# Performance work log

Hardware: AMD Instinct MI355X
Metric: run time of the kernel (lower is better)

Reference implementation:

```python
import jax, jax.numpy as jnp
import numpy as np

N = 50000   # total_ent
R = 16      # total_rel
D = 64      # emb_dim
F_IN = 128  # feat_in
L = 2       # gcn_layers
E = 100000  # edges per relation
EPS = 1e-12


def setup_inputs() -> dict:
    key = jax.random.key(0)
    ks = jax.random.split(key, 6)
    x = jax.random.normal(ks[0], (N, F_IN), jnp.float32)
    # xavier-uniform-ish scaled params
    ent_emb = jax.random.normal(ks[1], (F_IN, D), jnp.float32) * (1.0 / np.sqrt(F_IN))
    rel_trans = jax.random.normal(ks[2], (L, R, D, D), jnp.float32) * (1.0 / np.sqrt(D))
    edge_row = jax.random.randint(ks[3], (R, E), 0, N)
    edge_col = jax.random.randint(ks[4], (R, E), 0, N)
    edge_val = jax.random.uniform(ks[5], (R, E), jnp.float32)
    return dict(x=x, ent_emb=ent_emb, rel_trans=rel_trans,
                edge_row=edge_row, edge_col=edge_col, edge_val=edge_val)


def reference(x, ent_emb, rel_trans, edge_row, edge_col, edge_val):
    # emb = x @ ent_emb : [N, D]
    emb = x @ ent_emb

    def spmm_per_rel(emb):
        # per-relation sparse.mm: out[r, row] += val * emb[col]
        def one_rel(row, col, val):
            return jax.ops.segment_sum(val[:, None] * emb[col], row, num_segments=N)
        return jax.vmap(one_rel)(edge_row, edge_col, edge_val)  # [R, N, D]

    for l in range(L):
        emb_acc = spmm_per_rel(emb)                             # [R, N, D]
        # tmp[r] = (W_r @ emb_acc[r]^T)^T = emb_acc[r] @ W_r^T
        tmp = jnp.einsum('rne,rde->rnd', emb_acc, rel_trans[l])  # [R, N, D]
        emb = jax.nn.relu(tmp.sum(axis=0))                       # [N, D]

    # F.normalize(emb) : L2 over dim=1 with eps clamp
    norm = jnp.linalg.norm(emb, axis=1, keepdims=True)
    return emb / jnp.maximum(norm, EPS)
```

## Files before the change

### kernel.cpp

```cpp
#include <hip/hip_runtime.h>

#define Nn 50000
#define Rr 16
#define Dd 64
#define Fin 128
#define Ee 100000
#define NE (Rr * Ee)
#define NBKT 782
#define CB 256
#define EPB (NE / CB)
#define SCTOT (NBKT * CB)
#define SC_NB (SCTOT / 256)
#define NTILE (Nn / 16)

typedef __attribute__((ext_vector_type(8))) short short8;
typedef __attribute__((ext_vector_type(4))) float f32x4;
typedef unsigned short ushort_t;

__device__ inline ushort_t f2bf(float x) {
  union { float f; unsigned u; } v; v.f = x;
  unsigned u = v.u;
  return (ushort_t)((u + 0x7FFFu + ((u >> 16) & 1u)) >> 16);
}
__device__ inline float bf2f(ushort_t h) {
  union { unsigned u; float f; } v; v.u = ((unsigned)h) << 16; return v.f;
}

#define INIT_TILES 3125
#define INIT_NB 782
#define CONVW_NB 512
__global__ __launch_bounds__(256) void pre_k(const float* __restrict__ x,
                                             const float* __restrict__ ent,
                                             ushort_t* __restrict__ emb0,
                                             const float* __restrict__ rel,
                                             ushort_t* __restrict__ wbf,
                                             const int* __restrict__ erow,
                                             int* __restrict__ cnt) {
  __shared__ int lh[NBKT];
  int b = blockIdx.x;
  if (b < INIT_NB) {
    int wave = threadIdx.x >> 6, lane = threadIdx.x & 63;
    int nt = lane & 15, quad = lane >> 4;
    int tile = b * 4 + wave;
    if (tile >= INIT_TILES) return;
    const float* xr = x + ((long)tile * 16 + nt) * Fin + quad * 8;
    short8 afrag[4];
#pragma unroll
    for (int ks = 0; ks < 4; ++ks) {
      float4 p0 = *(const float4*)(xr + ks * 32);
      float4 p1 = *(const float4*)(xr + ks * 32 + 4);
      short8 a;
      a[0] = (short)f2bf(p0.x); a[1] = (short)f2bf(p0.y);
      a[2] = (short)f2bf(p0.z); a[3] = (short)f2bf(p0.w);
      a[4] = (short)f2bf(p1.x); a[5] = (short)f2bf(p1.y);
      a[6] = (short)f2bf(p1.z); a[7] = (short)f2bf(p1.w);
      afrag[ks] = a;
    }
    f32x4 acc[4];
#pragma unroll
    for (int dt = 0; dt < 4; ++dt) acc[dt] = (f32x4){0.f, 0.f, 0.f, 0.f};
#pragma unroll
    for (int ks = 0; ks < 4; ++ks) {
#pragma unroll
      for (int dt = 0; dt < 4; ++dt) {
        short8 bfr;
#pragma unroll
        for (int j = 0; j < 8; ++j)
          bfr[j] = (short)f2bf(ent[(unsigned)(ks * 32 + quad * 8 + j) * Dd + dt * 16 + nt]);
        acc[dt] = __builtin_amdgcn_mfma_f32_16x16x32_bf16(afrag[ks], bfr, acc[dt], 0, 0, 0);
      }
    }
#pragma unroll
    for (int dt = 0; dt < 4; ++dt)
#pragma unroll
      for (int reg = 0; reg < 4; ++reg) {
        int row = tile * 16 + quad * 4 + reg;
        emb0[(unsigned)row * Dd + dt * 16 + nt] = f2bf(acc[dt][reg]);
      }
  } else if (b < INIT_NB + CONVW_NB) {
    int i = (b - INIT_NB) * 256 + threadIdx.x;
    wbf[i] = f2bf(rel[i]);
  } else {
    int blk = b - INIT_NB - CONVW_NB;
    int t = threadIdx.x;
    for (int i = t; i < NBKT; i += 256) lh[i] = 0;
    __syncthreads();
    int r = blk >> 4;
    long gbase = (long)r * Ee + (blk & 15) * EPB;
    for (int i = t; i < EPB; i += 256)
      atomicAdd(&lh[erow[gbase + i] >> 6], 1);
    __syncthreads();
    for (int i = t; i < NBKT; i += 256) cnt[i * CB + blk] = lh[i];
  }
}

__global__ __launch_bounds__(256) void scan1_k(const int* __restrict__ cnt,
                                               int* __restrict__ bsum) {
  __shared__ int ls[256];
  int t = threadIdx.x;
  ls[t] = cnt[blockIdx.x * 256 + t];
  __syncthreads();
  for (int off = 128; off >= 1; off >>= 1) {
    if (t < off) ls[t] += ls[t + off];
    __syncthreads();
  }
  if (t == 0) bsum[blockIdx.x] = ls[0];
}

__global__ __launch_bounds__(1024) void scan2_k(int* __restrict__ bsum) {
  __shared__ int ls[1024];
  int t = threadIdx.x;
  int v = (t < SC_NB) ? bsum[t] : 0;
  ls[t] = v;
  __syncthreads();
  for (int off = 1; off < 1024; off <<= 1) {
    int x = (t >= off) ? ls[t - off] : 0;
    __syncthreads();
    ls[t] += x;
    __syncthreads();
  }
  if (t < SC_NB) bsum[t] = ls[t] - v;
}

__global__ __launch_bounds__(256) void scan3_k(int* __restrict__ cnt,
                                               const int* __restrict__ bsum,
                                               int* __restrict__ cbase,
                                               int* __restrict__ offs) {
  __shared__ int ls[256];
  int t = threadIdx.x, i = blockIdx.x * 256 + t;
  int v = cnt[i];
  ls[t] = v;
  __syncthreads();
  for (int off = 1; off < 256; off <<= 1) {
    int x = (t >= off) ? ls[t - off] : 0;
    __syncthreads();
    ls[t] += x;
    __syncthreads();
  }
  int excl = ls[t] - v + bsum[blockIdx.x];
  cnt[i] = excl;
  if (t == 0) cbase[blockIdx.x] = excl;
  if (i == SCTOT - 1) { cbase[NBKT] = NE; offs[Nn] = NE; }
}

__global__ __launch_bounds__(256) void place_k(const int* __restrict__ erow,
                                               const int* __restrict__ ecol,
                                               const float* __restrict__ ev,
                                               const int* __restrict__ base,
                                               uint2* __restrict__ ebkt) {
  __shared__ int lofs[NBKT];
  int blk = blockIdx.x, t = threadIdx.x;
  for (int i = t; i < NBKT; i += 256) lofs[i] = base[i * CB + blk];
  __syncthreads();
  int r = blk >> 4;
  long gbase = (long)r * Ee + (blk & 15) * EPB;
  for (int i = t; i < EPB; i += 256) {
    long idx = gbase + i;
    int row = erow[idx];
    int pos = atomicAdd(&lofs[row >> 6], 1);
    unsigned vb = f2bf(ev[idx]);
    ebkt[pos] = make_uint2(((unsigned)(row & 63) << 4) | (unsigned)r,
                           (vb << 16) | (unsigned)ecol[idx]);
  }
}

__global__ __launch_bounds__(256) void csort_k(const uint2* __restrict__ ebkt,
                                               const int* __restrict__ cbase,
                                               uint2* __restrict__ ed2,
                                               int* __restrict__ offs) {
  __shared__ int lcnt[64], lstart[64], lcur[64];
  int c = blockIdx.x, t = threadIdx.x;
  int s = cbase[c], e = cbase[c + 1];
  if (t < 64) lcnt[t] = 0;
  __syncthreads();
  for (int i = s + t; i < e; i += 256) atomicAdd(&lcnt[ebkt[i].x >> 4], 1);
  __syncthreads();
  if (t == 0) {
    int run = 0;
    for (int rl = 0; rl < 64; ++rl) {
      int cc = lcnt[rl];
      lstart[rl] = run; lcur[rl] = run; run += cc;
    }
  }
  __syncthreads();
  int nrow = Nn - c * 64; if (nrow > 64) nrow = 64;
  if (t < nrow) offs[c * 64 + t] = s + lstart[t];
  for (int i = s + t; i < e; i += 256) {
    uint2 q = ebkt[i];
    int pos = s + atomicAdd(&lcur[q.x >> 4], 1);
    ed2[pos] = make_uint2(q.x & 15u, q.y);
  }
}

__global__ __launch_bounds__(1024, 8) void fused_k(const ushort_t* __restrict__ emb,
                                                   const int* __restrict__ offs,
                                                   const uint2* __restrict__ ed2,
                                                   const ushort_t* __restrict__ wl,
                                                   ushort_t* __restrict__ embout,
                                                   float* __restrict__ finout,
                                                   int fin) {
  __shared__ ushort_t Zt[16 * 1024];
  __shared__ f32x4 ssred[4][4];
  const int lane = threadIdx.x & 63;
  const int wave = threadIdx.x >> 6;
  const int nt = lane & 15, quad = lane >> 4;
  const int tile = blockIdx.x;

  const int qb = quad << 3;
  const ushort_t* embnt = emb + nt;
  char* ztb = (char*)Zt;
  union AW { unsigned w[4]; short8 v; };

  {
    const int rl = wave;
    const int row = tile * 16 + rl;
    int off_l = (lane < 2) ? offs[row + lane] : 0;
    const int base = __shfl(off_l, 0, 64);
    const int len  = __shfl(off_l, 1, 64) - base;

    f32x4 acc[4];
#pragma unroll
    for (int dt = 0; dt < 4; ++dt) acc[dt] = (f32x4){0.f, 0.f, 0.f, 0.f};

    for (int c = 0; c < len; c += 32) {
      int p = c + (lane & 31);
      uint2 myed = (p < len) ? ed2[base + p] : make_uint2(0u, 0u);

      unsigned yw[4][4];
      unsigned aw[4];
#pragma unroll
      for (int jp = 0; jp < 4; ++jp) {
        unsigned q0 = (unsigned)__shfl((int)myed.y, qb + 2 * jp, 64);
        unsigned q1 = (unsigned)__shfl((int)myed.y, qb + 2 * jp + 1, 64);
        unsigned x0 = (unsigned)__shfl((int)myed.x, qb + 2 * jp, 64);
        unsigned x1 = (unsigned)__shfl((int)myed.x, qb + 2 * jp + 1, 64);
        const ushort_t* e0 = embnt + (q0 & 0xFFFFu) * 64u;
        const ushort_t* e1 = embnt + (q1 & 0xFFFFu) * 64u;
#pragma unroll
        for (int dt = 0; dt < 4; ++dt)
          yw[dt][jp] = (unsigned)e0[dt * 16] | ((unsigned)e1[dt * 16] << 16);
        unsigned t0 = (x0 == (unsigned)nt) ? (q0 >> 16) : 0u;
        unsigned t1 = (x1 == (unsigned)nt) ? (q1 >> 16) : 0u;
        aw[jp] = t0 | (t1 << 16);
      }

      AW af;
      af.w[0] = aw[0]; af.w[1] = aw[1]; af.w[2] = aw[2]; af.w[3] = aw[3];
#pragma unroll
      for (int dt = 0; dt < 4; ++dt) {
        AW bf;
#pragma unroll
        for (int jp = 0; jp < 4; ++jp) bf.w[jp] = yw[dt][jp];
        acc[dt] = __builtin_amdgcn_mfma_f32_16x16x32_bf16(af.v, bf.v, acc[dt], 0, 0, 0);
      }
    }

    const unsigned swz = (unsigned)((rl & 7) << 4);
    const unsigned rb = (unsigned)(rl * 2048 + quad * 512);
#pragma unroll
    for (int dt = 0; dt < 4; ++dt)
#pragma unroll
      for (int reg = 0; reg < 4; ++reg) {
        unsigned hv = (unsigned)f2bf(acc[dt][reg]);
        unsigned pv = (unsigned)__shfl_xor((int)hv, 1, 64);
        if ((nt & 1) == 0) {
          unsigned lg = rb + (unsigned)(reg * 128 + dt * 32 + nt * 2);
          *(unsigned*)(ztb + (lg ^ swz)) = hv | (pv << 16);
        }
      }
  }
  __syncthreads();

  const bool act = (wave < 4);
  f32x4 accO = (f32x4){0.f, 0.f, 0.f, 0.f};
  if (act) {
    const int s0 = nt * 2048 + (((quad    ) ^ (nt & 7)) << 4);
    const int s1 = nt * 2048 + (((quad + 4) ^ (nt & 7)) << 4);
    f32x4 accA = (f32x4){0.f, 0.f, 0.f, 0.f};
    f32x4 accB = (f32x4){0.f, 0.f, 0.f, 0.f};
#pragma unroll
    for (int r = 0; r < 16; r += 2) {
      const char* ab0 = ztb + r * 128;
      const char* ab1 = ztb + (r + 1) * 128;
      short8 a00 = *(const short8*)(ab0 + s0);
      short8 a01 = *(const short8*)(ab0 + s1);
      short8 a10 = *(const short8*)(ab1 + s0);
      short8 a11 = *(const short8*)(ab1 + s1);
      const ushort_t* bp0 = wl + (unsigned)(r * Dd + wave * 16 + nt) * Dd + qb;
      const ushort_t* bp1 = wl + (unsigned)((r + 1) * Dd + wave * 16 + nt) * Dd + qb;
      short8 b00 = *(const short8*)(bp0);
      short8 b01 = *(const short8*)(bp0 + 32);
      short8 b10 = *(const short8*)(bp1);
      short8 b11 = *(const short8*)(bp1 + 32);
      accA = __builtin_amdgcn_mfma_f32_16x16x32_bf16(a00, b00, accA, 0, 0, 0);
      accA = __builtin_amdgcn_mfma_f32_16x16x32_bf16(a01, b01, accA, 0, 0, 0);
      accB = __builtin_amdgcn_mfma_f32_16x16x32_bf16(a10, b10, accB, 0, 0, 0);
      accB = __builtin_amdgcn_mfma_f32_16x16x32_bf16(a11, b11, accB, 0, 0, 0);
    }
#pragma unroll
    for (int reg = 0; reg < 4; ++reg) accO[reg] = accA[reg] + accB[reg];
  }

  if (!fin) {
    if (act) {
#pragma unroll
      for (int reg = 0; reg < 4; ++reg) {
        int row = tile * 16 + quad * 4 + reg;
        embout[(unsigned)row * 64u + wave * 16 + nt] = f2bf(fmaxf(accO[reg], 0.f));
      }
    }
    return;
  }

  float v[4];
  if (act) {
    f32x4 ssq;
#pragma unroll
    for (int reg = 0; reg < 4; ++reg) {
      v[reg] = fmaxf(accO[reg], 0.f);
      ssq[reg] = v[reg] * v[reg];
    }
#pragma unroll
    for (int off = 8; off >= 1; off >>= 1)
#pragma unroll
      for (int reg = 0; reg < 4; ++reg)
        ssq[reg] += __shfl_xor(ssq[reg], off, 64);
    if (nt == 0) ssred[wave][quad] = ssq;
  }
  __syncthreads();
  if (act) {
    f32x4 t0 = ssred[0][quad], t1 = ssred[1][quad];
    f32x4 t2 = ssred[2][quad], t3 = ssred[3][quad];
#pragma unroll
    for (int reg = 0; reg < 4; ++reg) {
      float tot = t0[reg] + t1[reg] + t2[reg] + t3[reg];
      float sc = 1.f / fmaxf(sqrtf(tot), 1e-12f);
      int row = tile * 16 + quad * 4 + reg;
      finout[(unsigned)row * 64u + wave * 16 + nt] = v[reg] * sc;
    }
  }
}

extern "C" void kernel_launch(void* const* d_in, const int* in_sizes, int n_in,
                              void* d_out, int out_size, void* d_ws, size_t ws_size,
                              hipStream_t stream) {
  const float* x   = (const float*)d_in[0];
  const float* ent = (const float*)d_in[1];
  const float* rel = (const float*)d_in[2];
  const int* erow  = (const int*)d_in[3];
  const int* ecol  = (const int*)d_in[4];
  const float* ev  = (const float*)d_in[5];
  float* out = (float*)d_out;

  char* p = (char*)d_ws;
  ushort_t* emb_a = (ushort_t*)p;  p += (size_t)Nn * Dd * 2;
  ushort_t* emb_b = (ushort_t*)p;  p += (size_t)Nn * Dd * 2;
  ushort_t* wbf   = (ushort_t*)p;  p += (size_t)2 * Rr * Dd * Dd * 2;
  uint2* ebkt     = (uint2*)p;     p += (size_t)NE * 8;
  uint2* ed2      = (uint2*)p;     p += (size_t)NE * 8;
  int* cnt        = (int*)p;       p += (size_t)SCTOT * 4;
  int* bsum       = (int*)p;       p += (size_t)(SC_NB + 8) * 4;
  int* cbase      = (int*)p;       p += (size_t)(NBKT + 8) * 4;
  int* offs       = (int*)p;       p += (size_t)(Nn + 8) * 4;

  pre_k<<<INIT_NB + CONVW_NB + CB, 256, 0, stream>>>(
      x, ent, emb_a, rel, wbf, erow, cnt);
  scan1_k<<<SC_NB, 256, 0, stream>>>(cnt, bsum);
  scan2_k<<<1, 1024, 0, stream>>>(bsum);
  scan3_k<<<SC_NB, 256, 0, stream>>>(cnt, bsum, cbase, offs);
  place_k<<<CB, 256, 0, stream>>>(erow, ecol, ev, cnt, ebkt);
  csort_k<<<NBKT, 256, 0, stream>>>(ebkt, cbase, ed2, offs);

  fused_k<<<NTILE, 1024, 0, stream>>>(emb_a, offs, ed2, wbf, emb_b, nullptr, 0);
  fused_k<<<NTILE, 1024, 0, stream>>>(emb_b, offs, ed2,
                                      wbf + (size_t)Rr * Dd * Dd, nullptr, out, 1);
}
```

Baseline: 356.8 us.

## Shrink fused GCN block to four rows with zero-padded MFMA transform

The fused spmm+transform kernel now processes 4 rows per 256-thread block instead of 16 rows per 1024-thread block. The transform stage is restructured so all four waves run a 32-step K loop, with only 4 of 16 MFMA rows holding real data and the rest zero-padded. Smaller blocks are meant to reduce load imbalance from variable row lengths and idle waves at the barrier. In exchange, 3/4 of the transform MFMA work is wasted and the weight matrix is reloaded four times as often per row.

```diff
diff --git a/kernel.cpp b/kernel.cpp
--- a/kernel.cpp
+++ b/kernel.cpp
@@ -192,20 +192,18 @@
   }
 }
 
-__global__ __launch_bounds__(1024, 8) void fused_k(const ushort_t* __restrict__ emb,
-                                                   const int* __restrict__ offs,
-                                                   const uint2* __restrict__ ed2,
-                                                   const ushort_t* __restrict__ wl,
-                                                   ushort_t* __restrict__ embout,
-                                                   float* __restrict__ finout,
-                                                   int fin) {
-  __shared__ ushort_t Zt[16 * 1024];
-  __shared__ f32x4 ssred[4][4];
+__global__ __launch_bounds__(256) void fused_k(const ushort_t* __restrict__ emb,
+                                               const int* __restrict__ offs,
+                                               const uint2* __restrict__ ed2,
+                                               const ushort_t* __restrict__ wl,
+                                               ushort_t* __restrict__ embout,
+                                               float* __restrict__ finout,
+                                               int fin) {
+  __shared__ ushort_t Zt[4 * 1024];
+  __shared__ f32x4 ssred[4];
   const int lane = threadIdx.x & 63;
   const int wave = threadIdx.x >> 6;
   const int nt = lane & 15, quad = lane >> 4;
-  const int tile = blockIdx.x;
-
   const int qb = quad << 3;
   const ushort_t* embnt = emb + nt;
   char* ztb = (char*)Zt;
@@ -213,7 +211,7 @@
 
   {
     const int rl = wave;
-    const int row = tile * 16 + rl;
+    const int row = blockIdx.x * 4 + rl;
     int off_l = (lane < 2) ? offs[row + lane] : 0;
     const int base = __shfl(off_l, 0, 64);
     const int len  = __shfl(off_l, 1, 64) - base;
@@ -255,7 +253,7 @@
       }
     }
 
-    const unsigned swz = (unsigned)((rl & 7) << 4);
+    const unsigned swz = (unsigned)((rl & 3) << 4);
     const unsigned rb = (unsigned)(rl * 2048 + quad * 512);
 #pragma unroll
     for (int dt = 0; dt < 4; ++dt)
@@ -271,41 +269,26 @@
   }
   __syncthreads();
 
-  const bool act = (wave < 4);
+  const int arow = nt & 3;
+  const int abase = arow * 2048;
+  const unsigned aswz = (unsigned)(arow << 4);
+  const short8 zz = {0, 0, 0, 0, 0, 0, 0, 0};
   f32x4 accO = (f32x4){0.f, 0.f, 0.f, 0.f};
-  if (act) {
-    const int s0 = nt * 2048 + (((quad    ) ^ (nt & 7)) << 4);
-    const int s1 = nt * 2048 + (((quad + 4) ^ (nt & 7)) << 4);
-    f32x4 accA = (f32x4){0.f, 0.f, 0.f, 0.f};
-    f32x4 accB = (f32x4){0.f, 0.f, 0.f, 0.f};
-#pragma unroll
-    for (int r = 0; r < 16; r += 2) {
-      const char* ab0 = ztb + r * 128;
-      const char* ab1 = ztb + (r + 1) * 128;
-      short8 a00 = *(const short8*)(ab0 + s0);
-      short8 a01 = *(const short8*)(ab0 + s1);
-      short8 a10 = *(const short8*)(ab1 + s0);
-      short8 a11 = *(const short8*)(ab1 + s1);
-      const ushort_t* bp0 = wl + (unsigned)(r * Dd + wave * 16 + nt) * Dd + qb;
-      const ushort_t* bp1 = wl + (unsigned)((r + 1) * Dd + wave * 16 + nt) * Dd + qb;
-      short8 b00 = *(const short8*)(bp0);
-      short8 b01 = *(const short8*)(bp0 + 32);
-      short8 b10 = *(const short8*)(bp1);
-      short8 b11 = *(const short8*)(bp1 + 32);
-      accA = __builtin_amdgcn_mfma_f32_16x16x32_bf16(a00, b00, accA, 0, 0, 0);
-      accA = __builtin_amdgcn_mfma_f32_16x16x32_bf16(a01, b01, accA, 0, 0, 0);
-      accB = __builtin_amdgcn_mfma_f32_16x16x32_bf16(a10, b10, accB, 0, 0, 0);
-      accB = __builtin_amdgcn_mfma_f32_16x16x32_bf16(a11, b11, accB, 0, 0, 0);
-    }
-#pragma unroll
-    for (int reg = 0; reg < 4; ++reg) accO[reg] = accA[reg] + accB[reg];
+#pragma unroll
+  for (int kb = 0; kb < 32; ++kb) {
+    short8 af = *(const short8*)(ztb + abase + (((unsigned)(kb * 64 + quad * 16)) ^ aswz));
+    if (nt >= 4) af = zz;
+    const ushort_t* bp = wl + (unsigned)((kb >> 1) * 64 + wave * 16 + nt) * 64 +
+                         (kb & 1) * 32 + qb;
+    short8 bf = *(const short8*)bp;
+    accO = __builtin_amdgcn_mfma_f32_16x16x32_bf16(af, bf, accO, 0, 0, 0);
   }
 
   if (!fin) {
-    if (act) {
+    if (quad == 0) {
 #pragma unroll
       for (int reg = 0; reg < 4; ++reg) {
-        int row = tile * 16 + quad * 4 + reg;
+        int row = blockIdx.x * 4 + reg;
         embout[(unsigned)row * 64u + wave * 16 + nt] = f2bf(fmaxf(accO[reg], 0.f));
       }
     }
@@ -313,7 +296,7 @@
   }
 
   float v[4];
-  if (act) {
+  if (quad == 0) {
     f32x4 ssq;
 #pragma unroll
     for (int reg = 0; reg < 4; ++reg) {
@@ -325,17 +308,16 @@
 #pragma unroll
       for (int reg = 0; reg < 4; ++reg)
         ssq[reg] += __shfl_xor(ssq[reg], off, 64);
-    if (nt == 0) ssred[wave][quad] = ssq;
-  }
-  __syncthreads();
-  if (act) {
-    f32x4 t0 = ssred[0][quad], t1 = ssred[1][quad];
-    f32x4 t2 = ssred[2][quad], t3 = ssred[3][quad];
+    if (nt == 0) ssred[wave] = ssq;
+  }
+  __syncthreads();
+  if (quad == 0) {
+    f32x4 t0 = ssred[0], t1 = ssred[1], t2 = ssred[2], t3 = ssred[3];
 #pragma unroll
     for (int reg = 0; reg < 4; ++reg) {
       float tot = t0[reg] + t1[reg] + t2[reg] + t3[reg];
       float sc = 1.f / fmaxf(sqrtf(tot), 1e-12f);
-      int row = tile * 16 + quad * 4 + reg;
+      int row = blockIdx.x * 4 + reg;
       finout[(unsigned)row * 64u + wave * 16 + nt] = v[reg] * sc;
     }
   }
@@ -371,7 +353,7 @@
   place_k<<<CB, 256, 0, stream>>>(erow, ecol, ev, cnt, ebkt);
   csort_k<<<NBKT, 256, 0, stream>>>(ebkt, cbase, ed2, offs);
 
-  fused_k<<<NTILE, 1024, 0, stream>>>(emb_a, offs, ed2, wbf, emb_b, nullptr, 0);
-  fused_k<<<NTILE, 1024, 0, stream>>>(emb_b, offs, ed2,
+  fused_k<<<Nn / 4, 256, 0, stream>>>(emb_a, offs, ed2, wbf, emb_b, nullptr, 0);
+  fused_k<<<Nn / 4, 256, 0, stream>>>(emb_b, offs, ed2,
                                       wbf + (size_t)Rr * Dd * Dd, nullptr, out, 1);
 }
```

Result: slower. 555.8 us (+55.8%).
